# Optimization experiments

Hardware: AMD Instinct MI355X
Metric: run time of the kernel (lower is better)

Reference implementation:

```python
import jax, jax.numpy as jnp
import numpy as np

# --- batched state-vector quantum circuit sim: AngleEmbedding(RY) + BasicEntanglerLayers(RX + ring CNOT) ---

def _ry(state, theta, wire, n):
    # per-sample RY(theta) on `wire`; state: (B,) + (2,)*n complex
    ax = wire + 1
    c = jnp.cos(0.5 * theta).reshape((-1,) + (1,) * (n - 1)).astype(state.dtype)
    s = jnp.sin(0.5 * theta).reshape((-1,) + (1,) * (n - 1)).astype(state.dtype)
    s0 = jnp.take(state, 0, axis=ax)
    s1 = jnp.take(state, 1, axis=ax)
    return jnp.stack([c * s0 - s * s1, s * s0 + c * s1], axis=ax)

def _rx(state, theta, wire, n):
    # scalar RX(theta) on `wire` (shared weight across batch)
    ax = wire + 1
    c = jnp.cos(0.5 * theta).astype(state.dtype)
    s = (-1j * jnp.sin(0.5 * theta)).astype(state.dtype)
    s0 = jnp.take(state, 0, axis=ax)
    s1 = jnp.take(state, 1, axis=ax)
    return jnp.stack([c * s0 + s * s1, s * s0 + c * s1], axis=ax)

def _cnot(state, ctrl, tgt):
    ax_c = ctrl + 1
    s0 = jnp.take(state, 0, axis=ax_c)
    s1 = jnp.take(state, 1, axis=ax_c)
    ax_t = tgt + 1 if tgt < ctrl else tgt  # target axis index after removing ctrl axis
    s1 = jnp.flip(s1, axis=ax_t)
    return jnp.stack([s0, s1], axis=ax_c)

def _circuit(x_qin, qweights):
    # x_qin: (Bn, n) angles; qweights: (L, n)
    Bn, n = x_qin.shape
    state = jnp.zeros((Bn,) + (2,) * n, jnp.complex64)
    state = state.at[(slice(None),) + (0,) * n].set(1.0)
    for w in range(n):  # AngleEmbedding, rotation='Y'
        state = _ry(state, x_qin[:, w], w, n)
    for l in range(qweights.shape[0]):  # BasicEntanglerLayers
        for w in range(n):
            state = _rx(state, qweights[l, w], w, n)
        for w in range(n):
            state = _cnot(state, w, (w + 1) % n)
    probs = jnp.real(state * jnp.conj(state))
    outs = []
    for w in range(n):  # <Z_w> = P(bit_w=0) - P(bit_w=1)
        axes = tuple(a for a in range(1, n + 1) if a != w + 1)
        p = probs.sum(axis=axes)  # (Bn, 2)
        outs.append(p[:, 0] - p[:, 1])
    return jnp.stack(outs, axis=-1).astype(jnp.float32)


def setup_inputs() -> dict:
    key = jax.random.key(0)
    ks = jax.random.split(key, 9)
    B, N, H, NQ, L = 16, 1024, 256, 8, 2
    x = jax.random.normal(ks[0], (B, N, H), jnp.float32)
    norm_adj = jax.random.uniform(ks[1], (N, N), jnp.float32) / N
    Wg = jax.random.normal(ks[2], (H, H), jnp.float32) * 0.02
    bg = jax.random.normal(ks[3], (H,), jnp.float32) * 0.02
    Wpre = jax.random.normal(ks[4], (NQ, H), jnp.float32) * 0.05
    bpre = jax.random.normal(ks[5], (NQ,), jnp.float32) * 0.02
    qweights = jax.random.uniform(ks[6], (L, NQ), jnp.float32) * (2.0 * np.pi)
    Wpost = jax.random.normal(ks[7], (H, NQ), jnp.float32) * 0.1
    bpost = jax.random.normal(ks[8], (H,), jnp.float32) * 0.02
    return {"x": x, "norm_adj": norm_adj, "Wg": Wg, "bg": bg, "Wpre": Wpre,
            "bpre": bpre, "qweights": qweights, "Wpost": Wpost, "bpost": bpost}


def reference(x, norm_adj, Wg, bg, Wpre, bpre, qweights, Wpost, bpost):
    # GCN aggregation + GELU(Linear)  (dropout is identity in eval mode)
    x_agg = jnp.einsum('ij,bjh->bih', norm_adj, x)
    x_agg = jax.nn.gelu(x_agg @ Wg.T + bg, approximate=False)
    B, N, H = x_agg.shape
    x_flat = x_agg.reshape(B * N, H).astype(jnp.float32)
    x_qin = jnp.tanh(x_flat @ Wpre.T + bpre) * np.pi
    q_out = _circuit(x_qin, qweights)          # (B*N, n_qubits)
    out = (q_out @ Wpost.T + bpost).reshape(B, N, H)
    return out
```

## Files before the change

### kernel.cpp

```cpp
#include <hip/hip_runtime.h>
#include <math.h>

typedef __attribute__((ext_vector_type(8))) short bf16x8;
typedef _Float16 f16x8 __attribute__((ext_vector_type(8)));
typedef __attribute__((ext_vector_type(4))) float f32x4;

#define PI_F 3.14159265358979323846f

__device__ __forceinline__ unsigned short f2bf(float f) {
  unsigned int u = __float_as_uint(f);
  u += 0x7FFFu + ((u >> 16) & 1u);
  return (unsigned short)(u >> 16);
}

__device__ __forceinline__ float bf2f(unsigned short u) {
  return __uint_as_float(((unsigned int)u) << 16);
}

__device__ __forceinline__ void async_ld16(const unsigned short* g, unsigned short* l) {
  __builtin_amdgcn_global_load_lds(
      (const __attribute__((address_space(1))) void*)g,
      (__attribute__((address_space(3))) void*)l,
      16, 0, 0);
}

__device__ __forceinline__ float fast_erf(float x) {
  float a = fabsf(x);
  float t = 1.0f / fmaf(0.3275911f, a, 1.0f);
  float p = t * fmaf(t, fmaf(t, fmaf(t, fmaf(t, 1.061405429f, -1.453152027f),
                                     1.421413741f), -0.284496736f), 0.254829592f);
  float e = __expf(-a * a);
  float r = 1.0f - p * e;
  return copysignf(r, x);
}

__device__ __forceinline__ float fast_tanh(float a) {
  float e = __expf(2.0f * a);
  return 1.0f - 2.0f / (e + 1.0f);
}

template<int ML, int MR>
__device__ __forceinline__ void apply_rx(float re[4], float im[4], float c, float s) {
  float pr[4], pi[4];
  #pragma unroll
  for (int r = 0; r < 4; r++) {
    float vr = re[r ^ MR], vi = im[r ^ MR];
    if (ML) { vr = __shfl_xor(vr, ML, 64); vi = __shfl_xor(vi, ML, 64); }
    pr[r] = vr; pi[r] = vi;
  }
  #pragma unroll
  for (int r = 0; r < 4; r++) {
    re[r] = fmaf(c, re[r],  s * pi[r]);
    im[r] = fmaf(c, im[r], -s * pr[r]);
  }
}

__device__ __forceinline__ void fold_reduce8(float v[8], int L) {
  #pragma unroll
  for (int step = 0; step < 3; step++) {
    int d = 1 << step;
    int half = 4 >> step;
    bool hi = (L & d) != 0;
    #pragma unroll
    for (int w = 0; w < half; w++) {
      float send = hi ? v[w] : v[w + half];
      float recv = __shfl_xor(send, d, 64);
      v[w] = (hi ? v[w + half] : v[w]) + recv;
    }
  }
  v[0] += __shfl_xor(v[0], 8, 64);
  v[0] += __shfl_xor(v[0], 16, 64);
  v[0] += __shfl_xor(v[0], 32, 64);
}

__global__ __launch_bounds__(256)
void prep_kernel(const float* __restrict__ adj, unsigned short* __restrict__ adj_bf,
                 const float* __restrict__ Wg, unsigned short* __restrict__ Wg_bf,
                 const float* __restrict__ qw, unsigned short* __restrict__ Uri,
                 const float* __restrict__ Wpost, _Float16* __restrict__ Gt,
                 const float* __restrict__ x, unsigned short* __restrict__ xT) {
  __shared__ float smem[1056];
  int bid = blockIdx.x, t = threadIdx.x;
  if (bid < 1024) {
    int i = bid * 256 + t;
    float4 v = ((const float4*)adj)[i];
    ushort4 o; o.x = f2bf(v.x); o.y = f2bf(v.y); o.z = f2bf(v.z); o.w = f2bf(v.w);
    ((ushort4*)adj_bf)[i] = o;
  } else if (bid < 1088) {
    int i = (bid - 1024) * 256 + t;
    float4 v = ((const float4*)Wg)[i];
    ushort4 o; o.x = f2bf(v.x); o.y = f2bf(v.y); o.z = f2bf(v.z); o.w = f2bf(v.w);
    ((ushort4*)Wg_bf)[i] = o;
  } else if (bid < 1152) {
    if (t < 16) { smem[t] = cosf(0.5f * qw[t]); smem[16 + t] = sinf(0.5f * qw[t]); }
    __syncthreads();
    int wv = t >> 6, L = t & 63;
    int k = (bid - 1088) * 4 + wv;
    float re[4], im[4];
    #pragma unroll
    for (int r = 0; r < 4; r++) { re[r] = (r * 64 + L == k) ? 1.f : 0.f; im[r] = 0.f; }
    apply_rx<1, 0>(re, im, smem[0], smem[16]);
    apply_rx<2, 0>(re, im, smem[1], smem[17]);
    apply_rx<4, 0>(re, im, smem[2], smem[18]);
    apply_rx<8, 0>(re, im, smem[3], smem[19]);
    apply_rx<16, 0>(re, im, smem[4], smem[20]);
    apply_rx<32, 0>(re, im, smem[5], smem[21]);
    apply_rx<0, 1>(re, im, smem[6], smem[22]);
    apply_rx<0, 2>(re, im, smem[7], smem[23]);
    apply_rx<3, 0>(re, im, smem[8], smem[24]);
    apply_rx<6, 0>(re, im, smem[9], smem[25]);
    apply_rx<12, 0>(re, im, smem[10], smem[26]);
    apply_rx<24, 0>(re, im, smem[11], smem[27]);
    apply_rx<48, 0>(re, im, smem[12], smem[28]);
    apply_rx<32, 1>(re, im, smem[13], smem[29]);
    apply_rx<0, 3>(re, im, smem[14], smem[30]);
    apply_rx<3, 2>(re, im, smem[15], smem[31]);
    const int M[8] = {0xAB, 0xFD, 0xFA, 0xF5, 0xEA, 0xD5, 0xAA, 0x55};
    #pragma unroll
    for (int r = 0; r < 4; r++) {
      int n = 0;
      #pragma unroll
      for (int w = 0; w < 8; w++) {
        int bit = (__popc(L & (M[w] & 63)) ^ __popc((r << 6) & M[w])) & 1;
        n |= bit << w;
      }
      int row_re = ((n >> 4) << 5) + (n & 15);
      Uri[(size_t)row_re * 256 + k] = f2bf(re[r]);
      Uri[(size_t)(row_re + 16) * 256 + k] = f2bf(im[r]);
    }
  } else if (bid < 1168) {
    int tid = (bid - 1152) * 256 + t;
    int h = tid >> 4;
    int n0 = (tid & 15) << 4;
    float wv8[8];
    #pragma unroll
    for (int w = 0; w < 8; w++) wv8[w] = Wpost[h * 8 + w];
    #pragma unroll
    for (int j = 0; j < 16; j++) {
      int n = n0 + j;
      float sum = 0.f;
      #pragma unroll
      for (int w = 0; w < 8; w++) sum += ((n >> w) & 1) ? -wv8[w] : wv8[w];
      Gt[h * 256 + n] = (_Float16)sum;
    }
  } else {
    int tb = bid - 1168;
    int jt = tb & 31, ht = (tb >> 5) & 7, bb = tb >> 8;
    int tx = t & 31, ty = t >> 5;
    const float* xb = x + (size_t)bb * 1024 * 256;
    #pragma unroll
    for (int i = 0; i < 4; i++) {
      int j = jt * 32 + ty + i * 8;
      smem[(ty + i * 8) * 33 + tx] = xb[(size_t)j * 256 + ht * 32 + tx];
    }
    __syncthreads();
    unsigned short* xTb = xT + (size_t)bb * 256 * 1024;
    #pragma unroll
    for (int i = 0; i < 4; i++) {
      int h = ht * 32 + ty + i * 8;
      xTb[(size_t)h * 1024 + jt * 32 + tx] = f2bf(smem[tx * 33 + ty + i * 8]);
    }
  }
}

__global__ __launch_bounds__(256)
void gemm1_kernel(const unsigned short* __restrict__ A,
                  const unsigned short* __restrict__ Bt,
                  unsigned short* __restrict__ C,
                  int K, int tilesN, int ldC) {
  __shared__ unsigned short As[128 * 32];
  __shared__ unsigned short Bs[64 * 32];
  int rr  = blockIdx.x;
  int im  = rr / tilesN;
  int in_ = rr % tilesN;
  const unsigned short* Ab  = A  + (long long)im * 128 * K;
  const unsigned short* Btb = Bt + (long long)in_ * 64 * K;

  int t = threadIdx.x;
  int wv = t >> 6, lane = t & 63;
  int wm = wv >> 1, wn = wv & 1;
  int l15 = lane & 15, quad = lane >> 4;
  int row0 = t >> 2, cg = t & 3;

  f32x4 acc[4][2] = {};

  for (int kk = 0; kk < K; kk += 32) {
    __syncthreads();
    #pragma unroll
    for (int q = 0; q < 2; q++) {
      int row = row0 + q * 64;
      async_ld16(Ab + (long long)row * K + kk + cg * 8,
                 &As[(wv * 16 + q * 64) * 32]);
    }
    async_ld16(Btb + (long long)row0 * K + kk + cg * 8,
               &Bs[wv * 16 * 32]);
    __syncthreads();
    bf16x8 af[4], bfr[2];
    #pragma unroll
    for (int mt = 0; mt < 4; mt++)
      af[mt] = *(const bf16x8*)&As[(wm * 64 + mt * 16 + l15) * 32 + quad * 8];
    #pragma unroll
    for (int nt = 0; nt < 2; nt++)
      bfr[nt] = *(const bf16x8*)&Bs[(wn * 32 + nt * 16 + l15) * 32 + quad * 8];
    #pragma unroll
    for (int mt = 0; mt < 4; mt++)
      #pragma unroll
      for (int nt = 0; nt < 2; nt++)
        acc[mt][nt] = __builtin_amdgcn_mfma_f32_16x16x32_bf16(af[mt], bfr[nt], acc[mt][nt], 0, 0, 0);
  }

  int n0 = in_ * 64;
  #pragma unroll
  for (int mt = 0; mt < 4; mt++) {
    #pragma unroll
    for (int nt = 0; nt < 2; nt++) {
      int colg = n0 + wn * 32 + nt * 16 + l15;
      #pragma unroll
      for (int r = 0; r < 4; r++) {
        int rowg = im * 128 + wm * 64 + mt * 16 + quad * 4 + r;
        C[(size_t)rowg * ldC + colg] = f2bf(acc[mt][nt][r]);
      }
    }
  }
}

__global__ __launch_bounds__(256)
void gemm2p0_kernel(const unsigned short* __restrict__ xagg,
                    const unsigned short* __restrict__ Wg,
                    const float* __restrict__ bg,
                    const float* __restrict__ Wpre, const float* __restrict__ bpre,
                    unsigned short* __restrict__ P0) {
  __shared__ unsigned short As[32 * 32];
  __shared__ unsigned short Bs[256 * 32];
  __shared__ unsigned short gs[32 * 256];
  __shared__ float sWpre[2048];

  int t = threadIdx.x;
  int wv = t >> 6, lane = t & 63;
  int l15 = lane & 15, quad = lane >> 4;

  for (int i = t; i < 2048; i += 256) sWpre[i] = Wpre[i];

  const unsigned short* Ab = xagg + (size_t)blockIdx.x * 32 * 256;

  f32x4 acc[2][4] = {};
  for (int kk = 0; kk < 256; kk += 32) {
    __syncthreads();
    if (wv < 2)
      async_ld16(Ab + (size_t)(wv * 16 + (lane >> 2)) * 256 + kk + (lane & 3) * 8,
                 &As[(wv * 16) * 32]);
    #pragma unroll
    for (int rd = 0; rd < 4; rd++) {
      int n = wv * 64 + rd * 16 + (lane >> 2);
      async_ld16(Wg + (size_t)n * 256 + kk + (lane & 3) * 8,
                 &Bs[(wv * 64 + rd * 16) * 32]);
    }
    __syncthreads();
    bf16x8 af[2], bfr[4];
    #pragma unroll
    for (int mt = 0; mt < 2; mt++)
      af[mt] = *(const bf16x8*)&As[(mt * 16 + l15) * 32 + quad * 8];
    #pragma unroll
    for (int nt = 0; nt < 4; nt++)
      bfr[nt] = *(const bf16x8*)&Bs[(wv * 64 + nt * 16 + l15) * 32 + quad * 8];
    #pragma unroll
    for (int mt = 0; mt < 2; mt++)
      #pragma unroll
      for (int nt = 0; nt < 4; nt++)
        acc[mt][nt] = __builtin_amdgcn_mfma_f32_16x16x32_bf16(af[mt], bfr[nt], acc[mt][nt], 0, 0, 0);
  }

  #pragma unroll
  for (int mt = 0; mt < 2; mt++) {
    #pragma unroll
    for (int nt = 0; nt < 4; nt++) {
      int col = wv * 64 + nt * 16 + l15;
      float bgl = bg[col];
      #pragma unroll
      for (int r = 0; r < 4; r++) {
        int row = mt * 16 + quad * 4 + r;
        float v = acc[mt][nt][r] + bgl;
        v = 0.5f * v * (1.0f + fast_erf(v * 0.7071067811865475f));
        gs[row * 256 + col] = f2bf(v);
      }
    }
  }
  __syncthreads();

  #pragma unroll
  for (int rr = 0; rr < 8; rr++) {
    int row = wv * 8 + rr;
    ushort4 gu = *(const ushort4*)&gs[row * 256 + 4 * lane];
    float g0 = bf2f(gu.x), g1 = bf2f(gu.y), g2 = bf2f(gu.z), g3 = bf2f(gu.w);
    float ang[8];
    #pragma unroll
    for (int w = 0; w < 8; w++) {
      float4 wp = *(const float4*)&sWpre[w * 256 + 4 * lane];
      float a = g0 * wp.x;
      a = fmaf(g1, wp.y, a);
      a = fmaf(g2, wp.z, a);
      a = fmaf(g3, wp.w, a);
      ang[w] = a;
    }
    fold_reduce8(ang, lane);
    float angf[8];
    #pragma unroll
    for (int w = 0; w < 8; w++) {
      int src = ((w >> 2) & 1) | (w & 2) | ((w & 1) << 2);
      angf[w] = __shfl(ang[0], src, 64);
    }
    float cw[8], sw[8];
    #pragma unroll
    for (int w = 0; w < 8; w++) {
      float th = (0.5f * PI_F) * fast_tanh(angf[w] + bpre[w]);
      cw[w] = __cosf(th); sw[w] = __sinf(th);
    }
    float pl = 1.f;
    #pragma unroll
    for (int bbit = 0; bbit < 6; bbit++) pl *= ((lane >> bbit) & 1) ? sw[bbit + 2] : cw[bbit + 2];
    ushort4 o;
    o.x = f2bf(pl * cw[0] * cw[1]);
    o.y = f2bf(pl * sw[0] * cw[1]);
    o.z = f2bf(pl * cw[0] * sw[1]);
    o.w = f2bf(pl * sw[0] * sw[1]);
    size_t srow = (size_t)blockIdx.x * 32 + row;
    *(ushort4*)(P0 + srow * 256 + 4 * lane) = o;
  }
}

__global__ __launch_bounds__(256)
void qtail_kernel(const unsigned short* __restrict__ P0,
                  const unsigned short* __restrict__ Uri,
                  const _Float16* __restrict__ Gt,
                  const float* __restrict__ bpost,
                  float* __restrict__ out) {
  __shared__ unsigned short As[32 * 32];
  __shared__ unsigned short Bs[512 * 32];
  __shared__ _Float16 Ts[8 * 32 * 32];

  int t = threadIdx.x;
  int wv = t >> 6, lane = t & 63;
  int l15 = lane & 15, quad = lane >> 4;

  const unsigned short* Ab = P0 + (size_t)blockIdx.x * 32 * 256;

  f32x4 acc[2][8] = {};
  for (int kk = 0; kk < 256; kk += 32) {
    __syncthreads();
    if (wv < 2)
      async_ld16(Ab + (size_t)(wv * 16 + (lane >> 2)) * 256 + kk + (lane & 3) * 8,
                 &As[(wv * 16) * 32]);
    #pragma unroll
    for (int rd = 0; rd < 8; rd++) {
      int n = wv * 128 + rd * 16 + (lane >> 2);
      async_ld16(Uri + (size_t)n * 256 + kk + (lane & 3) * 8,
                 &Bs[(wv * 128 + rd * 16) * 32]);
    }
    __syncthreads();
    bf16x8 af[2], bfr[8];
    #pragma unroll
    for (int mt = 0; mt < 2; mt++)
      af[mt] = *(const bf16x8*)&As[(mt * 16 + l15) * 32 + quad * 8];
    #pragma unroll
    for (int nt = 0; nt < 8; nt++)
      bfr[nt] = *(const bf16x8*)&Bs[(wv * 128 + nt * 16 + l15) * 32 + quad * 8];
    #pragma unroll
    for (int mt = 0; mt < 2; mt++)
      #pragma unroll
      for (int nt = 0; nt < 8; nt++)
        acc[mt][nt] = __builtin_amdgcn_mfma_f32_16x16x32_bf16(af[mt], bfr[nt], acc[mt][nt], 0, 0, 0);
  }

  #pragma unroll
  for (int mt = 0; mt < 2; mt++) {
    #pragma unroll
    for (int p = 0; p < 4; p++) {
      int kb = wv * 2 + (p >> 1);
      int cip = (p & 1) * 16 + l15;
      #pragma unroll
      for (int r = 0; r < 4; r++) {
        int row = mt * 16 + quad * 4 + r;
        float tre = acc[mt][2 * p][r], tim = acc[mt][2 * p + 1][r];
        Ts[kb * 1024 + row * 32 + cip] = (_Float16)(tre * tre + tim * tim);
      }
    }
  }

  f32x4 acc2[2][4] = {};
  for (int kk = 0; kk < 256; kk += 32) {
    __syncthreads();
    #pragma unroll
    for (int rd = 0; rd < 4; rd++) {
      int h = wv * 64 + rd * 16 + (lane >> 2);
      async_ld16((const unsigned short*)Gt + (size_t)h * 256 + kk + (lane & 3) * 8,
                 &Bs[(wv * 64 + rd * 16) * 32]);
    }
    __syncthreads();
    f16x8 af[2], bfr[4];
    #pragma unroll
    for (int mt = 0; mt < 2; mt++)
      af[mt] = *(const f16x8*)&Ts[(kk >> 5) * 1024 + (mt * 16 + l15) * 32 + quad * 8];
    #pragma unroll
    for (int nt = 0; nt < 4; nt++)
      bfr[nt] = *(const f16x8*)&Bs[(wv * 64 + nt * 16 + l15) * 32 + quad * 8];
    #pragma unroll
    for (int mt = 0; mt < 2; mt++)
      #pragma unroll
      for (int nt = 0; nt < 4; nt++)
        acc2[mt][nt] = __builtin_amdgcn_mfma_f32_16x16x32_f16(af[mt], bfr[nt], acc2[mt][nt], 0, 0, 0);
  }

  #pragma unroll
  for (int mt = 0; mt < 2; mt++) {
    #pragma unroll
    for (int nt = 0; nt < 4; nt++) {
      int col = wv * 64 + nt * 16 + l15;
      float bp = bpost[col];
      #pragma unroll
      for (int r = 0; r < 4; r++) {
        int row = mt * 16 + quad * 4 + r;
        int s = blockIdx.x * 32 + row;
        int orow = (s & 15) * 1024 + (s >> 4);
        out[(size_t)orow * 256 + col] = acc2[mt][nt][r] + bp;
      }
    }
  }
}

extern "C" void kernel_launch(void* const* d_in, const int* in_sizes, int n_in,
                              void* d_out, int out_size, void* d_ws, size_t ws_size,
                              hipStream_t stream) {
  const float* x     = (const float*)d_in[0];
  const float* adj   = (const float*)d_in[1];
  const float* Wg    = (const float*)d_in[2];
  const float* bg    = (const float*)d_in[3];
  const float* Wpre  = (const float*)d_in[4];
  const float* bpre  = (const float*)d_in[5];
  const float* qw    = (const float*)d_in[6];
  const float* Wpost = (const float*)d_in[7];
  const float* bpost = (const float*)d_in[8];
  float* out = (float*)d_out;

  char* ws = (char*)d_ws;
  unsigned short* adj_bf  = (unsigned short*)(ws + 0);
  unsigned short* Wg_bf   = (unsigned short*)(ws + 2097152);
  unsigned short* xT_bf   = (unsigned short*)(ws + 2228224);
  unsigned short* xagg_bf = (unsigned short*)(ws + 10616832);
  unsigned short* P0      = (unsigned short*)(ws + 19005440);
  unsigned short* Uri     = (unsigned short*)(ws + 27394048);
  _Float16*       Gt      = (_Float16*)(ws + 27656192);

  prep_kernel<<<5264, 256, 0, stream>>>(adj, adj_bf, Wg, Wg_bf, qw, Uri,
                                        Wpost, Gt, x, xT_bf);

  gemm1_kernel<<<512, 256, 0, stream>>>(adj_bf, xT_bf, xagg_bf, 1024, 64, 4096);

  gemm2p0_kernel<<<512, 256, 0, stream>>>(xagg_bf, Wg_bf, bg, Wpre, bpre, P0);

  qtail_kernel<<<512, 256, 0, stream>>>(P0, Uri, Gt, bpost, out);
}
```

Baseline: 154.8 us.

## Fuse gemm2/P0 and quantum tail kernels via shared memory; double K-step in gemm1

Merges the GELU/P0-generation kernel with the quantum-tail kernel so the P0 amplitude tile stays in shared memory instead of making a round trip through global memory, and drops one launch. Separately, gemm1 now loads two 32-wide K slices per barrier pair, halving the synchronisation count. The fused kernel uses about 74KB of LDS per block, which may lower occupancy.

```diff
diff --git a/kernel.cpp b/kernel.cpp
--- a/kernel.cpp
+++ b/kernel.cpp
@@ -168,8 +168,8 @@
                   const unsigned short* __restrict__ Bt,
                   unsigned short* __restrict__ C,
                   int K, int tilesN, int ldC) {
-  __shared__ unsigned short As[128 * 32];
-  __shared__ unsigned short Bs[64 * 32];
+  __shared__ unsigned short As[2 * 128 * 32];
+  __shared__ unsigned short Bs[2 * 64 * 32];
   int rr  = blockIdx.x;
   int im  = rr / tilesN;
   int in_ = rr % tilesN;
@@ -180,33 +180,41 @@
   int wv = t >> 6, lane = t & 63;
   int wm = wv >> 1, wn = wv & 1;
   int l15 = lane & 15, quad = lane >> 4;
-  int row0 = t >> 2, cg = t & 3;
 
   f32x4 acc[4][2] = {};
 
-  for (int kk = 0; kk < K; kk += 32) {
-    __syncthreads();
-    #pragma unroll
-    for (int q = 0; q < 2; q++) {
-      int row = row0 + q * 64;
-      async_ld16(Ab + (long long)row * K + kk + cg * 8,
-                 &As[(wv * 16 + q * 64) * 32]);
-    }
-    async_ld16(Btb + (long long)row0 * K + kk + cg * 8,
-               &Bs[wv * 16 * 32]);
-    __syncthreads();
-    bf16x8 af[4], bfr[2];
-    #pragma unroll
-    for (int mt = 0; mt < 4; mt++)
-      af[mt] = *(const bf16x8*)&As[(wm * 64 + mt * 16 + l15) * 32 + quad * 8];
-    #pragma unroll
-    for (int nt = 0; nt < 2; nt++)
-      bfr[nt] = *(const bf16x8*)&Bs[(wn * 32 + nt * 16 + l15) * 32 + quad * 8];
-    #pragma unroll
-    for (int mt = 0; mt < 4; mt++)
+  for (int kk = 0; kk < K; kk += 64) {
+    __syncthreads();
+    #pragma unroll
+    for (int kb = 0; kb < 2; kb++) {
+      #pragma unroll
+      for (int q = 0; q < 2; q++) {
+        int ch = q * 256 + t;
+        async_ld16(Ab + (long long)(ch >> 2) * K + kk + kb * 32 + (ch & 3) * 8,
+                   &As[kb * 4096 + ch * 8]);
+      }
+      {
+        int ch = t;
+        async_ld16(Btb + (long long)(ch >> 2) * K + kk + kb * 32 + (ch & 3) * 8,
+                   &Bs[kb * 2048 + ch * 8]);
+      }
+    }
+    __syncthreads();
+    #pragma unroll
+    for (int kb = 0; kb < 2; kb++) {
+      bf16x8 af[4], bfr[2];
+      #pragma unroll
+      for (int mt = 0; mt < 4; mt++)
+        af[mt] = *(const bf16x8*)&As[kb * 4096 + (wm * 64 + mt * 16 + l15) * 32 + quad * 8];
       #pragma unroll
       for (int nt = 0; nt < 2; nt++)
-        acc[mt][nt] = __builtin_amdgcn_mfma_f32_16x16x32_bf16(af[mt], bfr[nt], acc[mt][nt], 0, 0, 0);
+        bfr[nt] = *(const bf16x8*)&Bs[kb * 2048 + (wn * 32 + nt * 16 + l15) * 32 + quad * 8];
+      #pragma unroll
+      for (int mt = 0; mt < 4; mt++)
+        #pragma unroll
+        for (int nt = 0; nt < 2; nt++)
+          acc[mt][nt] = __builtin_amdgcn_mfma_f32_16x16x32_bf16(af[mt], bfr[nt], acc[mt][nt], 0, 0, 0);
+    }
   }
 
   int n0 = in_ * 64;
@@ -225,15 +233,21 @@
 }
 
 __global__ __launch_bounds__(256)
-void gemm2p0_kernel(const unsigned short* __restrict__ xagg,
-                    const unsigned short* __restrict__ Wg,
-                    const float* __restrict__ bg,
-                    const float* __restrict__ Wpre, const float* __restrict__ bpre,
-                    unsigned short* __restrict__ P0) {
-  __shared__ unsigned short As[32 * 32];
-  __shared__ unsigned short Bs[256 * 32];
-  __shared__ unsigned short gs[32 * 256];
-  __shared__ float sWpre[2048];
+void qfused_kernel(const unsigned short* __restrict__ xagg,
+                   const unsigned short* __restrict__ Wg,
+                   const float* __restrict__ bg,
+                   const float* __restrict__ Wpre, const float* __restrict__ bpre,
+                   const unsigned short* __restrict__ Uri,
+                   const _Float16* __restrict__ Gt,
+                   const float* __restrict__ bpost,
+                   float* __restrict__ out) {
+  __shared__ __align__(16) char smemraw[75776];
+  unsigned short* As    = (unsigned short*)smemraw;
+  unsigned short* Bs    = (unsigned short*)(smemraw + 2048);
+  unsigned short* gs    = (unsigned short*)(smemraw + 34816);
+  _Float16*       Ts    = (_Float16*)(smemraw + 34816);
+  unsigned short* P0s   = (unsigned short*)(smemraw + 51200);
+  float*          sWpre = (float*)(smemraw + 67584);
 
   int t = threadIdx.x;
   int wv = t >> 6, lane = t & 63;
@@ -269,7 +283,6 @@
       for (int nt = 0; nt < 4; nt++)
         acc[mt][nt] = __builtin_amdgcn_mfma_f32_16x16x32_bf16(af[mt], bfr[nt], acc[mt][nt], 0, 0, 0);
   }
-
   #pragma unroll
   for (int mt = 0; mt < 2; mt++) {
     #pragma unroll
@@ -323,33 +336,12 @@
     o.y = f2bf(pl * sw[0] * cw[1]);
     o.z = f2bf(pl * cw[0] * sw[1]);
     o.w = f2bf(pl * sw[0] * sw[1]);
-    size_t srow = (size_t)blockIdx.x * 32 + row;
-    *(ushort4*)(P0 + srow * 256 + 4 * lane) = o;
-  }
-}
-
-__global__ __launch_bounds__(256)
-void qtail_kernel(const unsigned short* __restrict__ P0,
-                  const unsigned short* __restrict__ Uri,
-                  const _Float16* __restrict__ Gt,
-                  const float* __restrict__ bpost,
-                  float* __restrict__ out) {
-  __shared__ unsigned short As[32 * 32];
-  __shared__ unsigned short Bs[512 * 32];
-  __shared__ _Float16 Ts[8 * 32 * 32];
-
-  int t = threadIdx.x;
-  int wv = t >> 6, lane = t & 63;
-  int l15 = lane & 15, quad = lane >> 4;
-
-  const unsigned short* Ab = P0 + (size_t)blockIdx.x * 32 * 256;
-
-  f32x4 acc[2][8] = {};
+    *(ushort4*)&P0s[(lane >> 3) * 1024 + row * 32 + 4 * (lane & 7)] = o;
+  }
+
+  f32x4 acc1[2][8] = {};
   for (int kk = 0; kk < 256; kk += 32) {
     __syncthreads();
-    if (wv < 2)
-      async_ld16(Ab + (size_t)(wv * 16 + (lane >> 2)) * 256 + kk + (lane & 3) * 8,
-                 &As[(wv * 16) * 32]);
     #pragma unroll
     for (int rd = 0; rd < 8; rd++) {
       int n = wv * 128 + rd * 16 + (lane >> 2);
@@ -360,7 +352,7 @@
     bf16x8 af[2], bfr[8];
     #pragma unroll
     for (int mt = 0; mt < 2; mt++)
-      af[mt] = *(const bf16x8*)&As[(mt * 16 + l15) * 32 + quad * 8];
+      af[mt] = *(const bf16x8*)&P0s[(kk >> 5) * 1024 + (mt * 16 + l15) * 32 + quad * 8];
     #pragma unroll
     for (int nt = 0; nt < 8; nt++)
       bfr[nt] = *(const bf16x8*)&Bs[(wv * 128 + nt * 16 + l15) * 32 + quad * 8];
@@ -368,7 +360,7 @@
     for (int mt = 0; mt < 2; mt++)
       #pragma unroll
       for (int nt = 0; nt < 8; nt++)
-        acc[mt][nt] = __builtin_amdgcn_mfma_f32_16x16x32_bf16(af[mt], bfr[nt], acc[mt][nt], 0, 0, 0);
+        acc1[mt][nt] = __builtin_amdgcn_mfma_f32_16x16x32_bf16(af[mt], bfr[nt], acc1[mt][nt], 0, 0, 0);
   }
 
   #pragma unroll
@@ -380,7 +372,7 @@
       #pragma unroll
       for (int r = 0; r < 4; r++) {
         int row = mt * 16 + quad * 4 + r;
-        float tre = acc[mt][2 * p][r], tim = acc[mt][2 * p + 1][r];
+        float tre = acc1[mt][2 * p][r], tim = acc1[mt][2 * p + 1][r];
         Ts[kb * 1024 + row * 32 + cip] = (_Float16)(tre * tre + tim * tim);
       }
     }
@@ -446,16 +438,13 @@
   unsigned short* Wg_bf   = (unsigned short*)(ws + 2097152);
   unsigned short* xT_bf   = (unsigned short*)(ws + 2228224);
   unsigned short* xagg_bf = (unsigned short*)(ws + 10616832);
-  unsigned short* P0      = (unsigned short*)(ws + 19005440);
-  unsigned short* Uri     = (unsigned short*)(ws + 27394048);
-  _Float16*       Gt      = (_Float16*)(ws + 27656192);
+  unsigned short* Uri     = (unsigned short*)(ws + 19005440);
+  _Float16*       Gt      = (_Float16*)(ws + 19267584);
 
   prep_kernel<<<5264, 256, 0, stream>>>(adj, adj_bf, Wg, Wg_bf, qw, Uri,
                                         Wpost, Gt, x, xT_bf);
 
   gemm1_kernel<<<512, 256, 0, stream>>>(adj_bf, xT_bf, xagg_bf, 1024, 64, 4096);
 
-  gemm2p0_kernel<<<512, 256, 0, stream>>>(xagg_bf, Wg_bf, bg, Wpre, bpre, P0);
-
-  qtail_kernel<<<512, 256, 0, stream>>>(P0, Uri, Gt, bpost, out);
-}
+  qfused_kernel<<<512, 256, 0, stream>>>(xagg_bf, Wg_bf, bg, Wpre, bpre, Uri, Gt, bpost, out);
+}
```

After: 147.2 us. -4.9%, faster.
